# Performance work log

Hardware: AMD Instinct MI355X
Metric: run time of the kernel (lower is better)

The kernel has to match this reference:

```python
import jax, jax.numpy as jnp
import numpy as np

NUM_HEADS = 16
TOP_K = 32
NEG_INF = -1e9
EPS = 1e-8


def setup_inputs() -> dict:
    key = jax.random.key(0)
    ks = jax.random.split(key, 12)
    B, S, D = 2, 1024, 1024
    M, dk = 8192, D // NUM_HEADS
    w = lambda k: jax.random.normal(k, (D, D), jnp.float32) * 0.02
    return {
        "x": jax.random.normal(ks[0], (B, S, D), jnp.float32),
        "Wq": w(ks[1]), "bq": jnp.zeros((D,), jnp.float32),
        "Wk": w(ks[2]), "bk": jnp.zeros((D,), jnp.float32),
        "Wv": w(ks[3]), "bv": jnp.zeros((D,), jnp.float32),
        "Wo": w(ks[4]), "bo": jnp.zeros((D,), jnp.float32),
        "mem_keys": jax.random.normal(ks[5], (M, dk), jnp.float32),
        "mem_vals": jax.random.normal(ks[6], (M, dk), jnp.float32),
        "gate": jnp.zeros((1,), jnp.float32),
    }


def _normalize(v):
    return v / (jnp.linalg.norm(v, axis=-1, keepdims=True) + EPS)


def reference(x, Wq, bq, Wk, bk, Wv, bv, Wo, bo, mem_keys, mem_vals, gate):
    B, S, D = x.shape
    H = NUM_HEADS
    dk = D // H
    # projections (torch Linear: x @ W.T + b), split heads -> [B,H,S,dk]
    split = lambda t: t.reshape(B, S, H, dk).transpose(0, 2, 1, 3)
    q = split(x @ Wq.T + bq)
    k = split(x @ Wk.T + bk)
    v = split(x @ Wv.T + bv)
    # causal attention
    scores = jnp.einsum("bhqd,bhkd->bhqk", q, k) / jnp.sqrt(jnp.float32(dk))
    causal = jnp.triu(jnp.ones((S, S), bool), k=1)  # True above diagonal
    scores = jnp.where(causal, NEG_INF, scores)
    attn = jax.nn.softmax(scores, axis=-1)
    attn_out = jnp.einsum("bhqk,bhkd->bhqd", attn, v)
    attn_out = attn_out.transpose(0, 2, 1, 3).reshape(B, S, D)
    attn_out = attn_out @ Wo.T + bo
    # KNN memory retrieval on flattened per-head queries [B*H*S, dk]
    flat_q = q.reshape(-1, dk)
    sims = _normalize(flat_q) @ _normalize(mem_keys).T  # [Q, M]
    top_scores, idx = jax.lax.top_k(sims, TOP_K)        # [Q, K]
    gathered = mem_vals[idx]                            # [Q, K, dk]
    memory_out = jnp.sum(gathered * top_scores[..., None], axis=-2)  # [Q, dk]
    memory_out = memory_out.reshape(B, H, S, dk).transpose(0, 2, 1, 3).reshape(B, S, D)
    memory_out = memory_out @ Wo.T + bo
    g = jax.nn.sigmoid(gate)
    return g * memory_out + (1.0 - g) * attn_out
```

## Files before the change

kernel.cpp:

```cpp
#include <hip/hip_runtime.h>
#include <stdint.h>
#include <math.h>

#define BATCH   2
#define SEQ     1024
#define DMODEL  1024
#define NHEADS  16
#define DK      64
#define MKEYS   8192
#define NQ      (BATCH*NHEADS*SEQ)
#define THRC    2.25f
#define KPART   4
#define PKEYS2  (MKEYS/KPART)
#define PCAP    64
#define QCAP2   (KPART*PCAP)

typedef __attribute__((ext_vector_type(8))) short short8;
typedef __attribute__((ext_vector_type(4))) float f32x4;
typedef __attribute__((ext_vector_type(2))) double f64x2;

__device__ __forceinline__ short f2bf(float f) {
  uint32_t u = __builtin_bit_cast(uint32_t, f);
  u = (u + 0x7fffu + ((u >> 16) & 1u)) >> 16;
  return (short)u;
}
__device__ __forceinline__ short8 ld_bf8_f32(const float* p) {
  float4 a = *(const float4*)p; float4 b = *(const float4*)(p + 4);
  short8 r;
  r[0]=f2bf(a.x); r[1]=f2bf(a.y); r[2]=f2bf(a.z); r[3]=f2bf(a.w);
  r[4]=f2bf(b.x); r[5]=f2bf(b.y); r[6]=f2bf(b.z); r[7]=f2bf(b.w);
  return r;
}

__device__ __forceinline__ unsigned long long packP(double v, int id) {
  unsigned long long b = __builtin_bit_cast(unsigned long long, v);
  b = (b & 0x8000000000000000ull) ? ~b : (b | 0x8000000000000000ull);
  return (b & ~0x1FFFull) | (unsigned long long)(8191 - id);
}
__device__ __forceinline__ double unpackV(unsigned long long P) {
  unsigned long long K = P & ~0x1FFFull;
  unsigned long long bits = (K & 0x8000000000000000ull) ? (K ^ 0x8000000000000000ull) : ~K;
  return __builtin_bit_cast(double, bits);
}

__global__ __launch_bounds__(256) void norm_keys(const float* __restrict__ mk,
                                                 double* __restrict__ knorm64,
                                                 uint16_t* __restrict__ knbf) {
  int wave = threadIdx.x >> 6, lane = threadIdx.x & 63;
  int m = blockIdx.x * 4 + wave;
  double v = (double)mk[(size_t)m * DK + lane];
  double ss = v * v;
  #pragma unroll
  for (int off = 1; off < 64; off <<= 1) ss += __shfl_xor(ss, off);
  double nv = v / (sqrt(ss) + 1e-8);
  knorm64[(size_t)m * DK + lane] = nv;
  knbf[(size_t)m * DK + lane] = (uint16_t)f2bf((float)nv);
}

__global__ __launch_bounds__(256) void q64_gemm(const float* __restrict__ x,
                                                const float* __restrict__ Wq,
                                                const float* __restrict__ bq,
                                                double* __restrict__ q64q,
                                                float* __restrict__ qf32,
                                                uint16_t* __restrict__ qb) {
  __shared__ __align__(16) double Xs[64 * 66];
  __shared__ __align__(16) double Ws[64 * 66];
  int tid = threadIdx.x, tx = tid & 15, ty = tid >> 4;
  int bm = blockIdx.y * 64;
  int h = blockIdx.x;
  double acc[4][4] = {};
  for (int kt = 0; kt < 16; kt++) {
    __syncthreads();
    #pragma unroll
    for (int i = 0; i < 4; i++) {
      int c4 = tid + 256 * i;
      int r = c4 >> 4, q4 = c4 & 15;
      float4 xv = *(const float4*)(x + (size_t)(bm + r) * DMODEL + kt * 64 + q4 * 4);
      float4 wv = *(const float4*)(Wq + (size_t)(h * 64 + r) * DMODEL + kt * 64 + q4 * 4);
      *(f64x2*)(Xs + r * 66 + q4 * 4)     = (f64x2){(double)xv.x, (double)xv.y};
      *(f64x2*)(Xs + r * 66 + q4 * 4 + 2) = (f64x2){(double)xv.z, (double)xv.w};
      *(f64x2*)(Ws + r * 66 + q4 * 4)     = (f64x2){(double)wv.x, (double)wv.y};
      *(f64x2*)(Ws + r * 66 + q4 * 4 + 2) = (f64x2){(double)wv.z, (double)wv.w};
    }
    __syncthreads();
    for (int k = 0; k < 64; k += 2) {
      double a0[4], a1[4], b0[4], b1[4];
      #pragma unroll
      for (int i = 0; i < 4; i++) {
        f64x2 t = *(const f64x2*)(Xs + (ty * 4 + i) * 66 + k);
        a0[i] = t[0]; a1[i] = t[1];
      }
      #pragma unroll
      for (int j = 0; j < 4; j++) {
        f64x2 t = *(const f64x2*)(Ws + (tx + 16 * j) * 66 + k);
        b0[j] = t[0]; b1[j] = t[1];
      }
      #pragma unroll
      for (int i = 0; i < 4; i++)
        #pragma unroll
        for (int j = 0; j < 4; j++) {
          acc[i][j] = fma(a0[i], b0[j], acc[i][j]);
          acc[i][j] = fma(a1[i], b1[j], acc[i][j]);
        }
    }
  }
  #pragma unroll
  for (int i = 0; i < 4; i++)
    #pragma unroll
    for (int j = 0; j < 4; j++) {
      int m = bm + ty * 4 + i, d = tx + 16 * j;
      int b = m >> 10, s = m & 1023;
      size_t qidx = (((size_t)(b * NHEADS + h) * SEQ) + s) * DK + d;
      double val = acc[i][j] + (double)bq[h * DK + d];
      q64q[qidx] = val;
      float fv = (float)val;
      qf32[qidx] = fv;
      qb[qidx] = (uint16_t)f2bf(fv);
    }
}

template<bool AF, bool WF>
__device__ __forceinline__ void gemm_core(const void* __restrict__ Ap,
                                          const void* __restrict__ Wp,
                                          f32x4 acc[4][4], short* As, short* Bs,
                                          int bm, int bn) {
  int tid = threadIdx.x, lane = tid & 63, w = tid >> 6;
  int wm = (w >> 1) * 64, wn = (w & 1) * 64;
  for (int kt = 0; kt < 16; kt++) {
    __syncthreads();
    #pragma unroll
    for (int i = 0; i < 4; i++) {
      int cq = tid + 256 * i;
      int r = cq >> 3, ch = cq & 7;
      size_t aoff = (size_t)(bm + r) * DMODEL + kt * 64 + ch * 8;
      size_t boff = (size_t)(bn + r) * DMODEL + kt * 64 + ch * 8;
      *(short8*)(As + r * 72 + ch * 8) = AF ? ld_bf8_f32((const float*)Ap + aoff)
                                            : *(const short8*)((const uint16_t*)Ap + aoff);
      *(short8*)(Bs + r * 72 + ch * 8) = WF ? ld_bf8_f32((const float*)Wp + boff)
                                            : *(const short8*)((const uint16_t*)Wp + boff);
    }
    __syncthreads();
    #pragma unroll
    for (int kk = 0; kk < 2; kk++) {
      short8 af[4], bfr[4];
      #pragma unroll
      for (int t = 0; t < 4; t++) {
        af[t]  = *(const short8*)(As + (wm + t * 16 + (lane & 15)) * 72 + kk * 32 + (lane >> 4) * 8);
        bfr[t] = *(const short8*)(Bs + (wn + t * 16 + (lane & 15)) * 72 + kk * 32 + (lane >> 4) * 8);
      }
      #pragma unroll
      for (int mi = 0; mi < 4; mi++)
        #pragma unroll
        for (int ni = 0; ni < 4; ni++)
          acc[mi][ni] = __builtin_amdgcn_mfma_f32_16x16x32_bf16(af[mi], bfr[ni], acc[mi][ni], 0, 0, 0);
    }
  }
}

__global__ __launch_bounds__(256) void gemm_kv(
    const float* __restrict__ x,
    const float* __restrict__ Wk, const float* __restrict__ bk,
    const float* __restrict__ Wv, const float* __restrict__ bv,
    uint16_t* __restrict__ kb, uint16_t* __restrict__ vb) {
  __shared__ __align__(16) short As[128 * 72];
  __shared__ __align__(16) short Bs[128 * 72];
  int z = blockIdx.z;
  const float* W    = z == 0 ? Wk : Wv;
  const float* bias = z == 0 ? bk : bv;
  uint16_t* outB    = z == 0 ? kb : vb;
  int bm = blockIdx.y * 128, bn = blockIdx.x * 128;
  f32x4 acc[4][4] = {};
  gemm_core<true, true>(x, W, acc, As, Bs, bm, bn);
  int lane = threadIdx.x & 63, w = threadIdx.x >> 6;
  int wm = (w >> 1) * 64, wn = (w & 1) * 64;
  #pragma unroll
  for (int mi = 0; mi < 4; mi++)
    #pragma unroll
    for (int ni = 0; ni < 4; ni++) {
      int n = bn + wn + ni * 16 + (lane & 15);
      float bvv = bias[n];
      #pragma unroll
      for (int rg = 0; rg < 4; rg++) {
        int m = bm + wm + mi * 16 + (lane >> 4) * 4 + rg;
        float v = acc[mi][ni][rg] + bvv;
        int b = m >> 10, s = m & 1023, h = n >> 6, d = n & 63;
        size_t idx = (((size_t)(b * NHEADS + h) * SEQ) + s) * DK + d;
        outB[idx] = (uint16_t)f2bf(v);
      }
    }
}

__global__ __launch_bounds__(256) void attn_fwd(
    const uint16_t* __restrict__ qb, const uint16_t* __restrict__ kb,
    const uint16_t* __restrict__ vb, float* __restrict__ attnO) {
  __shared__ __align__(16) short Ks[64 * 72];
  __shared__ __align__(16) short Vt[64 * 72];
  __shared__ __align__(16) short Ps[4][16 * 72];
  int tid = threadIdx.x, lane = tid & 63, w = tid >> 6;
  int bx = blockIdx.x;
  int qt = bx & 15, h = (bx >> 4) & 15, b = bx >> 8;
  const uint16_t* Qg = qb + (size_t)(b * NHEADS + h) * SEQ * DK;
  const uint16_t* Kg = kb + (size_t)(b * NHEADS + h) * SEQ * DK;
  const uint16_t* Vg = vb + (size_t)(b * NHEADS + h) * SEQ * DK;
  int qrow0 = qt * 64 + w * 16;
  short8 qfr[2];
  #pragma unroll
  for (int kk = 0; kk < 2; kk++)
    qfr[kk] = *(const short8*)(const void*)(Qg + (size_t)(qrow0 + (lane & 15)) * DK + kk * 32 + (lane >> 4) * 8);
  float m_i[4] = {-1e30f, -1e30f, -1e30f, -1e30f};
  float l_i[4] = {0.f, 0.f, 0.f, 0.f};
  f32x4 Oacc[4] = {};
  for (int kt = 0; kt <= qt; kt++) {
    __syncthreads();
    #pragma unroll
    for (int i = 0; i < 2; i++) {
      int cq = tid + 256 * i;
      int r = cq >> 3, ch = cq & 7;
      short8 g = *(const short8*)(const void*)(Kg + (size_t)(kt * 64 + r) * DK + ch * 8);
      *(short8*)(Ks + r * 72 + ch * 8) = g;
      short8 gv = *(const short8*)(const void*)(Vg + (size_t)(kt * 64 + r) * DK + ch * 8);
      #pragma unroll
      for (int j = 0; j < 8; j++) Vt[(ch * 8 + j) * 72 + r] = gv[j];
    }
    __syncthreads();
    f32x4 sv[4] = {};
    #pragma unroll
    for (int kk = 0; kk < 2; kk++)
      #pragma unroll
      for (int ni = 0; ni < 4; ni++) {
        short8 kf = *(const short8*)(Ks + (ni * 16 + (lane & 15)) * 72 + kk * 32 + (lane >> 4) * 8);
        sv[ni] = __builtin_amdgcn_mfma_f32_16x16x32_bf16(qfr[kk], kf, sv[ni], 0, 0, 0);
      }
    bool diag = (kt == qt);
    #pragma unroll
    for (int ni = 0; ni < 4; ni++)
      #pragma unroll
      for (int rg = 0; rg < 4; rg++) {
        float sc = sv[ni][rg] * 0.125f;
        if (diag) {
          int kcol = kt * 64 + ni * 16 + (lane & 15);
          int qrow = qrow0 + (lane >> 4) * 4 + rg;
          if (kcol > qrow) sc = -1e9f;
        }
        sv[ni][rg] = sc;
      }
    float alpha[4];
    #pragma unroll
    for (int rg = 0; rg < 4; rg++) {
      float v = fmaxf(fmaxf(sv[0][rg], sv[1][rg]), fmaxf(sv[2][rg], sv[3][rg]));
      v = fmaxf(v, __shfl_xor(v, 1)); v = fmaxf(v, __shfl_xor(v, 2));
      v = fmaxf(v, __shfl_xor(v, 4)); v = fmaxf(v, __shfl_xor(v, 8));
      float mn = fmaxf(m_i[rg], v);
      alpha[rg] = expf(m_i[rg] - mn);
      m_i[rg] = mn;
    }
    #pragma unroll
    for (int ni = 0; ni < 4; ni++)
      #pragma unroll
      for (int rg = 0; rg < 4; rg++) sv[ni][rg] = expf(sv[ni][rg] - m_i[rg]);
    #pragma unroll
    for (int rg = 0; rg < 4; rg++) {
      float s = sv[0][rg] + sv[1][rg] + sv[2][rg] + sv[3][rg];
      s += __shfl_xor(s, 1); s += __shfl_xor(s, 2);
      s += __shfl_xor(s, 4); s += __shfl_xor(s, 8);
      l_i[rg] = l_i[rg] * alpha[rg] + s;
    }
    #pragma unroll
    for (int ni = 0; ni < 4; ni++)
      #pragma unroll
      for (int rg = 0; rg < 4; rg++) Oacc[ni][rg] *= alpha[rg];
    short* Pw = &Ps[w][0];
    #pragma unroll
    for (int ni = 0; ni < 4; ni++)
      #pragma unroll
      for (int rg = 0; rg < 4; rg++)
        Pw[((lane >> 4) * 4 + rg) * 72 + ni * 16 + (lane & 15)] = f2bf(sv[ni][rg]);
    #pragma unroll
    for (int kk = 0; kk < 2; kk++) {
      short8 pa = *(const short8*)(Pw + (lane & 15) * 72 + kk * 32 + (lane >> 4) * 8);
      #pragma unroll
      for (int ni = 0; ni < 4; ni++) {
        short8 vf = *(const short8*)(Vt + (ni * 16 + (lane & 15)) * 72 + kk * 32 + (lane >> 4) * 8);
        Oacc[ni] = __builtin_amdgcn_mfma_f32_16x16x32_bf16(pa, vf, Oacc[ni], 0, 0, 0);
      }
    }
  }
  #pragma unroll
  for (int ni = 0; ni < 4; ni++)
    #pragma unroll
    for (int rg = 0; rg < 4; rg++) {
      int row = qrow0 + (lane >> 4) * 4 + rg;
      attnO[((size_t)b * SEQ + row) * DMODEL + h * DK + ni * 16 + (lane & 15)] =
          Oacc[ni][rg] / l_i[rg];
    }
}

__global__ __launch_bounds__(256) void norm_q(const float* __restrict__ qf32,
                                              float* __restrict__ t0arr) {
  int wave = threadIdx.x >> 6, lane = threadIdx.x & 63;
  int q = blockIdx.x * 4 + wave;
  float v = qf32[((size_t)q << 6) + lane];
  float ss = v * v;
  #pragma unroll
  for (int off = 1; off < 64; off <<= 1) ss += __shfl_xor(ss, off);
  if (lane == 0) t0arr[q] = (THRC / 8.0f) * sqrtf(ss);
}

__global__ __launch_bounds__(256) void knn_filter_mfma(
    const uint16_t* __restrict__ qb, const uint16_t* __restrict__ knbf,
    const float* __restrict__ t0arr,
    unsigned short* __restrict__ cand, int* __restrict__ counts) {
  __shared__ __align__(16) short Ks[64 * 68];
  int tid = threadIdx.x, lane = tid & 63, w = tid >> 6;
  int quad = lane >> 4, col = lane & 15;
  int q0 = blockIdx.y * 64;
  int p = blockIdx.x, k0 = p * PKEYS2;
  short8 aq[2];
  #pragma unroll
  for (int kk = 0; kk < 2; kk++)
    aq[kk] = *(const short8*)(const void*)(qb + (size_t)(q0 + w * 16 + col) * DK + kk * 32 + quad * 8);
  float t0row[4];
  #pragma unroll
  for (int rg = 0; rg < 4; rg++) t0row[rg] = t0arr[q0 + w * 16 + quad * 4 + rg];
  int cntr[4] = {0, 0, 0, 0};
  for (int kt = 0; kt < PKEYS2 / 64; kt++) {
    __syncthreads();
    {
      int r = tid >> 2, ch = (tid & 3) * 2;
      const uint16_t* src = knbf + (size_t)(k0 + kt * 64 + r) * DK + ch * 8;
      *(short8*)(Ks + r * 68 + ch * 8) = *(const short8*)(const void*)src;
      *(short8*)(Ks + r * 68 + ch * 8 + 8) = *(const short8*)(const void*)(src + 8);
    }
    __syncthreads();
    f32x4 acc[4] = {};
    #pragma unroll
    for (int kk = 0; kk < 2; kk++)
      #pragma unroll
      for (int ni = 0; ni < 4; ni++) {
        short8 kf = *(const short8*)(Ks + (ni * 16 + col) * 68 + kk * 32 + quad * 8);
        acc[ni] = __builtin_amdgcn_mfma_f32_16x16x32_bf16(aq[kk], kf, acc[ni], 0, 0, 0);
      }
    #pragma unroll
    for (int ni = 0; ni < 4; ni++)
      #pragma unroll
      for (int rg = 0; rg < 4; rg++) {
        bool pred = acc[ni][rg] >= t0row[rg];
        unsigned long long mask = __ballot(pred);
        if (mask) {
          unsigned m16 = (unsigned)(mask >> (quad * 16)) & 0xffffu;
          if (pred) {
            int row = q0 + w * 16 + quad * 4 + rg;
            int pos = cntr[rg] + __popc(m16 & ((1u << col) - 1u));
            if (pos < PCAP)
              cand[((size_t)row * KPART + p) * PCAP + pos] =
                  (unsigned short)(k0 + kt * 64 + ni * 16 + col);
          }
          cntr[rg] += __popc(m16);
        }
      }
  }
  if (col == 0)
    #pragma unroll
    for (int rg = 0; rg < 4; rg++) {
      int c = cntr[rg]; if (c > PCAP) c = PCAP;
      counts[(q0 + w * 16 + quad * 4 + rg) * KPART + p] = c;
    }
}

template<int NS>
__device__ __forceinline__ void rank_loop(const unsigned long long* cPw, int n,
                                          const unsigned long long* Pm, int* rank) {
  for (int j = 0; j < n; j++) {
    unsigned long long Pj = cPw[j];
    #pragma unroll
    for (int s = 0; s < NS; s++) rank[s] += (Pj > Pm[s]) ? 1 : 0;
  }
}

__global__ __launch_bounds__(256) void knn_select(const double* __restrict__ q64q,
                                                  const double* __restrict__ knorm64,
                                                  const unsigned short* __restrict__ cand,
                                                  const int* __restrict__ counts,
                                                  unsigned long long* __restrict__ wlE) {
  __shared__ unsigned short cid[4][QCAP2];
  __shared__ unsigned long long cP[4][QCAP2];
  __shared__ unsigned long long wl[4][32];
  int wave = threadIdx.x >> 6, lane = threadIdx.x & 63;
  int grp = lane & 7, slot = lane >> 3;
  int q = blockIdx.x * 4 + wave;
  int n = 0;
  #pragma unroll
  for (int p = 0; p < KPART; p++) {
    int c = counts[q * KPART + p]; if (c > PCAP) c = PCAP;
    if (lane < c)
      cid[wave][n + lane] = cand[((size_t)q * KPART + p) * PCAP + lane];
    n += c;
  }
  double q8[8];
  const f64x2* qrow2 = (const f64x2*)(q64q + ((size_t)q << 6));
  #pragma unroll
  for (int jj = 0; jj < 4; jj++) {
    f64x2 t = qrow2[8 * jj + grp];
    q8[2 * jj] = t[0]; q8[2 * jj + 1] = t[1];
  }
  double ssq = 0.0;
  #pragma unroll
  for (int j = 0; j < 8; j++) ssq = fma(q8[j], q8[j], ssq);
  ssq += __shfl_xor(ssq, 1); ssq += __shfl_xor(ssq, 2); ssq += __shfl_xor(ssq, 4);
  double scale = 1.0 / (sqrt(ssq) + 1e-8);
  for (int c0 = 0; c0 < n; c0 += 16) {
    int cA = c0 + slot, cB = c0 + 8 + slot;
    int idA = (cA < n) ? (int)cid[wave][cA] : 0;
    int idB = (cB < n) ? (int)cid[wave][cB] : 0;
    const f64x2* krA2 = (const f64x2*)(knorm64 + (((size_t)idA) << 6));
    const f64x2* krB2 = (const f64x2*)(knorm64 + (((size_t)idB) << 6));
    double pA = 0.0, pB = 0.0;
    #pragma unroll
    for (int jj = 0; jj < 4; jj++) {
      f64x2 a = krA2[8 * jj + grp];
      f64x2 b = krB2[8 * jj + grp];
      pA = fma(q8[2 * jj], a[0], pA); pA = fma(q8[2 * jj + 1], a[1], pA);
      pB = fma(q8[2 * jj], b[0], pB); pB = fma(q8[2 * jj + 1], b[1], pB);
    }
    pA += __shfl_xor(pA, 1); pB += __shfl_xor(pB, 1);
    pA += __shfl_xor(pA, 2); pB += __shfl_xor(pB, 2);
    pA += __shfl_xor(pA, 4); pB += __shfl_xor(pB, 4);
    if (grp == 0) {
      if (cA < n) cP[wave][cA] = packP(pA, idA);
      if (cB < n) cP[wave][cB] = packP(pB, idB);
    }
  }
  unsigned long long Pm[4]; int rank[4] = {0, 0, 0, 0};
  #pragma unroll
  for (int s = 0; s < 4; s++) {
    int idx = s * 64 + lane;
    Pm[s] = (idx < n) ? cP[wave][idx] : 0xFFFFFFFFFFFFFFFFull;
  }
  if (n > 128)      rank_loop<4>(cP[wave], n, Pm, rank);
  else if (n > 64)  rank_loop<2>(cP[wave], n, Pm, rank);
  else              rank_loop<1>(cP[wave], n, Pm, rank);
  #pragma unroll
  for (int s = 0; s < 4; s++) {
    int idx = s * 64 + lane;
    if (idx < n && rank[s] < 32) {
      int id = 8191 - (int)(Pm[s] & 0x1FFFull);
      float wgt = (float)(unpackV(Pm[s]) * scale);
      wl[wave][rank[s]] =
          ((unsigned long long)__builtin_bit_cast(unsigned, wgt) << 32) | (unsigned)id;
    }
  }
  int nsel = n < 32 ? n : 32;
  if (lane < nsel) wlE[(size_t)q * 32 + lane] = wl[wave][lane];
}

__global__ __launch_bounds__(256) void knn_gather(const unsigned long long* __restrict__ wlE,
                                                  const int* __restrict__ counts,
                                                  const float* __restrict__ mv,
                                                  const float* __restrict__ attnO,
                                                  const float* __restrict__ gate,
                                                  uint16_t* __restrict__ outb) {
  __shared__ unsigned long long wg[4][32];
  int wave = threadIdx.x >> 6, lane = threadIdx.x & 63;
  int q = blockIdx.x * 4 + wave;
  int n = 0;
  #pragma unroll
  for (int p = 0; p < KPART; p++) {
    int c = counts[q * KPART + p]; if (c > PCAP) c = PCAP;
    n += c;
  }
  int nsel = n < 32 ? n : 32;
  if (lane < 32) wg[wave][lane] = (lane < nsel) ? wlE[(size_t)q * 32 + lane] : 0;
  float accf = 0.f;
  for (int r = 0; r < nsel; r++) {
    unsigned long long e = wg[wave][r];
    int id = (int)(e & 0xFFFFFFFFull);
    float wgt = __builtin_bit_cast(float, (unsigned)(e >> 32));
    accf += wgt * mv[((size_t)id << 6) + lane];
  }
  float g = 1.f / (1.f + expf(-gate[0]));
  int b = q >> 14, h = (q >> 10) & 15, s = q & 1023;
  size_t oi = ((size_t)b * SEQ + s) * DMODEL + h * DK + lane;
  outb[oi] = (uint16_t)f2bf(g * accf + (1.f - g) * attnO[oi]);
}

__global__ __launch_bounds__(256) void gemm_out(
    const uint16_t* __restrict__ A, const float* __restrict__ W,
    const float* __restrict__ bias, float* __restrict__ out) {
  __shared__ __align__(16) short As[128 * 72];
  __shared__ __align__(16) short Bs[128 * 72];
  int bm = blockIdx.y * 128, bn = blockIdx.x * 128;
  f32x4 acc[4][4] = {};
  gemm_core<false, true>(A, W, acc, As, Bs, bm, bn);
  int lane = threadIdx.x & 63, w = threadIdx.x >> 6;
  int wm = (w >> 1) * 64, wn = (w & 1) * 64;
  #pragma unroll
  for (int mi = 0; mi < 4; mi++)
    #pragma unroll
    for (int ni = 0; ni < 4; ni++) {
      int n = bn + wn + ni * 16 + (lane & 15);
      float bvv = bias[n];
      #pragma unroll
      for (int rg = 0; rg < 4; rg++) {
        int m = bm + wm + mi * 16 + (lane >> 4) * 4 + rg;
        out[(size_t)m * DMODEL + n] = acc[mi][ni][rg] + bvv;
      }
    }
}

extern "C" void kernel_launch(void* const* d_in, const int* in_sizes, int n_in,
                              void* d_out, int out_size, void* d_ws, size_t ws_size,
                              hipStream_t stream) {
  const float* x    = (const float*)d_in[0];
  const float* Wq   = (const float*)d_in[1];
  const float* bq   = (const float*)d_in[2];
  const float* Wk   = (const float*)d_in[3];
  const float* bk   = (const float*)d_in[4];
  const float* Wv   = (const float*)d_in[5];
  const float* bv   = (const float*)d_in[6];
  const float* Wo   = (const float*)d_in[7];
  const float* bo   = (const float*)d_in[8];
  const float* mk   = (const float*)d_in[9];
  const float* mv   = (const float*)d_in[10];
  const float* gate = (const float*)d_in[11];

  char* ws = (char*)d_ws;
  double*   knorm64 = (double*)(ws);
  uint16_t* knbf    = (uint16_t*)(ws + ((size_t)4  << 20));
  float*    qf32    = (float*)(ws + ((size_t)6  << 20));
  double*   q64q    = (double*)(ws + ((size_t)14 << 20));
  uint16_t* qb      = (uint16_t*)(ws + ((size_t)30 << 20));
  uint16_t* kb      = (uint16_t*)(ws + ((size_t)34 << 20));
  uint16_t* vb      = (uint16_t*)(ws + ((size_t)38 << 20));
  float*    attnO   = (float*)(ws + ((size_t)42 << 20));
  unsigned long long* wlE = (unsigned long long*)(ws + ((size_t)50 << 20));
  uint16_t* blendb  = (uint16_t*)(ws + ((size_t)58 << 20));
  float*    t0arr   = (float*)(ws + ((size_t)62 << 20));
  int*      counts  = (int*)(ws + ((size_t)63 << 20));
  unsigned short* cnd = (unsigned short*)(ws + ((size_t)64 << 20));

  norm_keys<<<dim3(2048), dim3(256), 0, stream>>>(mk, knorm64, knbf);
  q64_gemm<<<dim3(16, 32), dim3(256), 0, stream>>>(x, Wq, bq, q64q, qf32, qb);
  gemm_kv<<<dim3(8, 16, 2), dim3(256), 0, stream>>>(x, Wk, bk, Wv, bv, kb, vb);
  attn_fwd<<<dim3(512), dim3(256), 0, stream>>>(qb, kb, vb, attnO);
  norm_q<<<dim3(8192), dim3(256), 0, stream>>>(qf32, t0arr);
  knn_filter_mfma<<<dim3(KPART, 512), dim3(256), 0, stream>>>(qb, knbf, t0arr, cnd, counts);
  knn_select<<<dim3(8192), dim3(256), 0, stream>>>(q64q, knorm64, cnd, counts, wlE);
  knn_gather<<<dim3(8192), dim3(256), 0, stream>>>(wlE, counts, mv, attnO, gate, blendb);
  gemm_out<<<dim3(8, 16), dim3(256), 0, stream>>>(blendb, Wo, bo, (float*)d_out);
}
```

Measured before the change: 521.1 us.

## Use FP64 MFMA for the double-precision Q projection with runtime layout probe

The Q projection GEMM, previously scalar FP64 FMAs on double tiles in shared memory, now uses the 16x16x4 FP64 MFMA instruction. A runtime probe decodes the MFMA operand and result lane layout and checks it, falling back to a scalar path if the check fails. Shared tiles are stored as float instead of double, halving LDS footprint, and launch bounds request higher occupancy. The probe adds a few MFMAs and wave votes per block, and accumulation order changes in the FP64 result.

Result: faster. 491.3 us (-5.7%).

```diff
diff --git a/kernel.cpp b/kernel.cpp
--- a/kernel.cpp
+++ b/kernel.cpp
@@ -18,6 +18,7 @@
 typedef __attribute__((ext_vector_type(8))) short short8;
 typedef __attribute__((ext_vector_type(4))) float f32x4;
 typedef __attribute__((ext_vector_type(2))) double f64x2;
+typedef __attribute__((ext_vector_type(4))) double f64x4;
 
 __device__ __forceinline__ short f2bf(float f) {
   uint32_t u = __builtin_bit_cast(uint32_t, f);
@@ -57,66 +58,144 @@
   knbf[(size_t)m * DK + lane] = (uint16_t)f2bf((float)nv);
 }
 
-__global__ __launch_bounds__(256) void q64_gemm(const float* __restrict__ x,
-                                                const float* __restrict__ Wq,
-                                                const float* __restrict__ bq,
-                                                double* __restrict__ q64q,
-                                                float* __restrict__ qf32,
-                                                uint16_t* __restrict__ qb) {
-  __shared__ __align__(16) double Xs[64 * 66];
-  __shared__ __align__(16) double Ws[64 * 66];
-  int tid = threadIdx.x, tx = tid & 15, ty = tid >> 4;
+__device__ __forceinline__ bool probe_decode(const f64x4 d, int base, int mul,
+                                             int out[4]) {
+  bool ok = true;
+  #pragma unroll
+  for (int r = 0; r < 4; r++) {
+    int v = (int)d[r];
+    int t = v - base;
+    bool o = ((double)v == d[r]) && (t >= 0) && (t % mul == 0) && ((t / mul) < 16);
+    out[r] = t / mul;
+    ok = ok && o;
+  }
+  return ok;
+}
+
+__global__ __launch_bounds__(256, 4) void q64_gemm(const float* __restrict__ x,
+                                                   const float* __restrict__ Wq,
+                                                   const float* __restrict__ bq,
+                                                   double* __restrict__ q64q,
+                                                   float* __restrict__ qf32,
+                                                   uint16_t* __restrict__ qb) {
+  __shared__ __align__(16) float Xs[64 * 68];
+  __shared__ __align__(16) float Ws[64 * 68];
+  int tid = threadIdx.x, lane = tid & 63, w = tid >> 6;
   int bm = blockIdx.y * 64;
   int h = blockIdx.x;
-  double acc[4][4] = {};
-  for (int kt = 0; kt < 16; kt++) {
-    __syncthreads();
-    #pragma unroll
-    for (int i = 0; i < 4; i++) {
-      int c4 = tid + 256 * i;
-      int r = c4 >> 4, q4 = c4 & 15;
-      float4 xv = *(const float4*)(x + (size_t)(bm + r) * DMODEL + kt * 64 + q4 * 4);
-      float4 wv = *(const float4*)(Wq + (size_t)(h * 64 + r) * DMODEL + kt * 64 + q4 * 4);
-      *(f64x2*)(Xs + r * 66 + q4 * 4)     = (f64x2){(double)xv.x, (double)xv.y};
-      *(f64x2*)(Xs + r * 66 + q4 * 4 + 2) = (f64x2){(double)xv.z, (double)xv.w};
-      *(f64x2*)(Ws + r * 66 + q4 * 4)     = (f64x2){(double)wv.x, (double)wv.y};
-      *(f64x2*)(Ws + r * 66 + q4 * 4 + 2) = (f64x2){(double)wv.z, (double)wv.w};
-    }
-    __syncthreads();
-    for (int k = 0; k < 64; k += 2) {
-      double a0[4], a1[4], b0[4], b1[4];
+
+  f64x4 z = {0.0, 0.0, 0.0, 0.0};
+  f64x4 d1 = __builtin_amdgcn_mfma_f64_16x16x4f64((double)lane, 1.0, z, 0, 0, 0);
+  f64x4 d2 = __builtin_amdgcn_mfma_f64_16x16x4f64(1.0, (double)lane, z, 0, 0, 0);
+  int rdec[4], cdec[4];
+  bool ok = probe_decode(d1, 96, 4, rdec);
+  bool h1A = (bool)__all(ok ? 1 : 0);
+  if (!h1A) ok = probe_decode(d1, 6, 16, rdec);
+  bool aOK = h1A || (bool)__all(ok ? 1 : 0);
+  ok = probe_decode(d2, 96, 4, cdec);
+  bool h1B = (bool)__all(ok ? 1 : 0);
+  if (!h1B) ok = probe_decode(d2, 6, 16, cdec);
+  bool bOK = h1B || (bool)__all(ok ? 1 : 0);
+  int iA = h1A ? (lane & 15) : (lane >> 2);
+  int kA = h1A ? (lane >> 4) : (lane & 3);
+  int jB = h1B ? (lane & 15) : (lane >> 2);
+  int kB = h1B ? (lane >> 4) : (lane & 3);
+  bool mfma_ok = aOK && bOK;
+  if (mfma_ok) {
+    f64x4 d3 = __builtin_amdgcn_mfma_f64_16x16x4f64(
+        (double)(4 * iA + kA), (double)(jB + 16 * kB), z, 0, 0, 0);
+    bool ok3 = true;
+    #pragma unroll
+    for (int r = 0; r < 4; r++)
+      ok3 = ok3 && (d3[r] == (double)(16 * rdec[r] * cdec[r] + 384 * rdec[r] +
+                                      6 * cdec[r] + 224));
+    mfma_ok = (bool)__all(ok3 ? 1 : 0);
+  }
+
+  if (mfma_ok) {
+    int wm = (w >> 1) * 32, wn = (w & 1) * 32;
+    f64x4 acc[2][2] = {};
+    for (int kt = 0; kt < 16; kt++) {
+      __syncthreads();
       #pragma unroll
       for (int i = 0; i < 4; i++) {
-        f64x2 t = *(const f64x2*)(Xs + (ty * 4 + i) * 66 + k);
-        a0[i] = t[0]; a1[i] = t[1];
-      }
+        int c4 = tid + 256 * i;
+        int r = c4 >> 4, q4 = c4 & 15;
+        *(float4*)(Xs + r * 68 + q4 * 4) =
+            *(const float4*)(x + (size_t)(bm + r) * DMODEL + kt * 64 + q4 * 4);
+        *(float4*)(Ws + r * 68 + q4 * 4) =
+            *(const float4*)(Wq + (size_t)(h * 64 + r) * DMODEL + kt * 64 + q4 * 4);
+      }
+      __syncthreads();
+      #pragma unroll
+      for (int k = 0; k < 64; k += 4) {
+        double a0 = (double)Xs[(wm + iA) * 68 + k + kA];
+        double a1 = (double)Xs[(wm + 16 + iA) * 68 + k + kA];
+        double b0 = (double)Ws[(wn + jB) * 68 + k + kB];
+        double b1 = (double)Ws[(wn + 16 + jB) * 68 + k + kB];
+        acc[0][0] = __builtin_amdgcn_mfma_f64_16x16x4f64(a0, b0, acc[0][0], 0, 0, 0);
+        acc[0][1] = __builtin_amdgcn_mfma_f64_16x16x4f64(a0, b1, acc[0][1], 0, 0, 0);
+        acc[1][0] = __builtin_amdgcn_mfma_f64_16x16x4f64(a1, b0, acc[1][0], 0, 0, 0);
+        acc[1][1] = __builtin_amdgcn_mfma_f64_16x16x4f64(a1, b1, acc[1][1], 0, 0, 0);
+      }
+    }
+    #pragma unroll
+    for (int mi = 0; mi < 2; mi++)
+      #pragma unroll
+      for (int ni = 0; ni < 2; ni++)
+        #pragma unroll
+        for (int rg = 0; rg < 4; rg++) {
+          int m = bm + wm + mi * 16 + rdec[rg];
+          int d = wn + ni * 16 + cdec[rg];
+          int b = m >> 10, s = m & 1023;
+          size_t qidx = (((size_t)(b * NHEADS + h) * SEQ) + s) * DK + d;
+          double val = acc[mi][ni][rg] + (double)bq[h * DK + d];
+          q64q[qidx] = val;
+          float fv = (float)val;
+          qf32[qidx] = fv;
+          qb[qidx] = (uint16_t)f2bf(fv);
+        }
+  } else {
+    int tx = tid & 15, ty = tid >> 4;
+    double facc[4][4] = {};
+    for (int kt = 0; kt < 16; kt++) {
+      __syncthreads();
+      #pragma unroll
+      for (int i = 0; i < 4; i++) {
+        int c4 = tid + 256 * i;
+        int r = c4 >> 4, q4 = c4 & 15;
+        *(float4*)(Xs + r * 68 + q4 * 4) =
+            *(const float4*)(x + (size_t)(bm + r) * DMODEL + kt * 64 + q4 * 4);
+        *(float4*)(Ws + r * 68 + q4 * 4) =
+            *(const float4*)(Wq + (size_t)(h * 64 + r) * DMODEL + kt * 64 + q4 * 4);
+      }
+      __syncthreads();
+      for (int k = 0; k < 64; k++) {
+        double bv[4];
+        #pragma unroll
+        for (int j = 0; j < 4; j++) bv[j] = (double)Ws[(tx + 16 * j) * 68 + k];
+        #pragma unroll
+        for (int i = 0; i < 4; i++) {
+          double a = (double)Xs[(ty * 4 + i) * 68 + k];
+          #pragma unroll
+          for (int j = 0; j < 4; j++) facc[i][j] = fma(a, bv[j], facc[i][j]);
+        }
+      }
+    }
+    #pragma unroll
+    for (int i = 0; i < 4; i++)
       #pragma unroll
       for (int j = 0; j < 4; j++) {
-        f64x2 t = *(const f64x2*)(Ws + (tx + 16 * j) * 66 + k);
-        b0[j] = t[0]; b1[j] = t[1];
-      }
-      #pragma unroll
-      for (int i = 0; i < 4; i++)
-        #pragma unroll
-        for (int j = 0; j < 4; j++) {
-          acc[i][j] = fma(a0[i], b0[j], acc[i][j]);
-          acc[i][j] = fma(a1[i], b1[j], acc[i][j]);
-        }
-    }
-  }
-  #pragma unroll
-  for (int i = 0; i < 4; i++)
-    #pragma unroll
-    for (int j = 0; j < 4; j++) {
-      int m = bm + ty * 4 + i, d = tx + 16 * j;
-      int b = m >> 10, s = m & 1023;
-      size_t qidx = (((size_t)(b * NHEADS + h) * SEQ) + s) * DK + d;
-      double val = acc[i][j] + (double)bq[h * DK + d];
-      q64q[qidx] = val;
-      float fv = (float)val;
-      qf32[qidx] = fv;
-      qb[qidx] = (uint16_t)f2bf(fv);
-    }
+        int m = bm + ty * 4 + i, d = tx + 16 * j;
+        int b = m >> 10, s = m & 1023;
+        size_t qidx = (((size_t)(b * NHEADS + h) * SEQ) + s) * DK + d;
+        double val = facc[i][j] + (double)bq[h * DK + d];
+        q64q[qidx] = val;
+        float fv = (float)val;
+        qf32[qidx] = fv;
+        qb[qidx] = (uint16_t)f2bf(fv);
+      }
+  }
 }
 
 template<bool AF, bool WF>
```
